# Optimization experiments

Hardware: AMD Instinct MI355X
Metric: run time of the kernel (lower is better)

## Reference

```python
import jax, jax.numpy as jnp
import numpy as np

B, C, D, H, W = 8, 1, 160, 160, 160
SPATIAL_AXES = (2, 3, 4)  # axial, coronal, sagittal map to dims D, H, W


def setup_inputs() -> dict:
    key = jax.random.key(0)
    k1, _ = jax.random.split(key)
    x = jax.random.normal(k1, (B, C, D, H, W), dtype=jnp.float32)
    log_sigma = jnp.zeros((3,), dtype=jnp.float32)  # log(initial_sigma=1.0)
    return {"x": x, "log_sigma": log_sigma}


def reference(x, log_sigma):
    # For each spatial axis: adjacent-slice diff, squared distance summed over
    # channel + remaining spatial dims (per batch, per slice-pair), RBF kernel,
    # then -mean over (batch, slice-pairs). Equivalent to the original
    # sum_i(-mean_b(k_i)) / (n_slices - 1) since mean is linear.
    sigma = jnp.exp(log_sigma)
    total = jnp.float32(0.0)
    for i, ax in enumerate(SPATIAL_AXES):
        d = jnp.diff(x, axis=ax)  # [B, C, ...] with S-1 along ax
        reduce_dims = tuple(a for a in range(5) if a not in (0, ax))
        sq = jnp.sum(d * d, axis=reduce_dims)  # [B, S-1]
        k = jnp.exp(-sq / (2.0 * sigma[i] ** 2))
        total = total + (-jnp.mean(k))
    return total / jnp.float32(len(SPATIAL_AXES))
```

## Files before the change

kernel.cpp:

```cpp
#include <hip/hip_runtime.h>


constexpr int Wd4 = 40;
constexpr int SLICE4 = 6400;
constexpr long BSTR4 = 160L * 6400;
constexpr int NB = 8;
constexpr int ND = 160;
constexpr int NPAIR = 159;
constexpr int NKEY = 3 * NB * NPAIR;
constexpr int BLK_STRIDE = 384;
constexpr int NBLK = NB * ND;
constexpr int PART_OFF = NBLK * BLK_STRIDE;
constexpr int NFIN = 60;

__device__ __forceinline__ float sq4(const float4& a, const float4& c) {
    float e0 = a.x - c.x, e1 = a.y - c.y, e2 = a.z - c.z, e3 = a.w - c.w;
    return e0 * e0 + e1 * e1 + e2 * e2 + e3 * e3;
}

__global__ __launch_bounds__(320) void diff3_kernel(const float* __restrict__ x,
                                                    float* __restrict__ ws) {
    __shared__ float ldsH[20][321];
    __shared__ float accW[160];
    __shared__ float accD;

    const int t = threadIdx.x;
    const int bid = blockIdx.x;
    const int xcd = bid & 7;
    const int idx = bid >> 3;
    const int b = idx / 20;
    const int d = xcd * 20 + idx % 20;
    const bool hasNext = (d < 159);

    const int c4 = t % 40;
    const int r0 = t / 40;
    const bool sOK = (c4 < 39);

    if (t < 160) accW[t] = 0.f;
    if (t == 0)  accD = 0.f;
    __syncthreads();

    const float4* curp = (const float4*)x + (size_t)b * BSTR4 + (size_t)d * SLICE4 + t;
    const float4* nxtp = curp + SLICE4;

    float aW0 = 0.f, aW1 = 0.f, aW2 = 0.f, aW3 = 0.f;
    float aD = 0.f;
    float aH[20];
#pragma unroll
    for (int j = 0; j < 20; ++j) aH[j] = 0.f;

#pragma unroll
    for (int j = 0; j < 20; ++j) {
        const float4 v = curp[320 * j];
        float4 nv;
        if (hasNext) nv = nxtp[320 * j];
        float4 hv;
        const bool hok = (j < 19) || (r0 < 7);
        if (hok) hv = curp[320 * j + Wd4];
        float sb = 0.f;
        if (sOK) sb = ((const float*)(curp + 320 * j))[4];

        float dw;
        dw = v.y - v.x; aW0 += dw * dw;
        dw = v.z - v.y; aW1 += dw * dw;
        dw = v.w - v.z; aW2 += dw * dw;
        if (sOK) { dw = sb - v.w; aW3 += dw * dw; }
        if (hok) aH[j] += sq4(hv, v);
        if (hasNext) aD += sq4(nv, v);
    }

#pragma unroll
    for (int j = 0; j < 20; ++j) ldsH[j][t] = aH[j];
    atomicAdd(&accW[c4 * 4 + 0], aW0);
    atomicAdd(&accW[c4 * 4 + 1], aW1);
    atomicAdd(&accW[c4 * 4 + 2], aW2);
    if (sOK) atomicAdd(&accW[c4 * 4 + 3], aW3);
    if (hasNext) {
        for (int off = 32; off > 0; off >>= 1) aD += __shfl_down(aD, off, 64);
        if ((t & 63) == 0) atomicAdd(&accD, aD);
    }
    __syncthreads();

    float* slot = ws + (size_t)(b * ND + d) * BLK_STRIDE;
    if (t == 0) slot[0] = accD;
    if (t < 160) {
        const int r = t;
        float s = 0.f;
        const float* src = &ldsH[r >> 3][(r & 7) * 40];
        for (int i = 0; i < 40; ++i) s += src[i];
        slot[1 + r] = s;
    }
    if (t >= 160) slot[161 + (t - 160)] = accW[t - 160];
}

__global__ __launch_bounds__(64) void reduce_kernel(const float* __restrict__ ws,
                                                    const float* __restrict__ log_sigma,
                                                    float* __restrict__ part) {
    const int gk = blockIdx.x * 64 + threadIdx.x;
    float kv = 0.f;
    if (gk < NKEY) {
        const int a = gk / (NB * NPAIR);
        const int rem = gk % (NB * NPAIR);
        const int b = rem / NPAIR;
        const int key = rem % NPAIR;
        const float f = -0.5f * expf(-2.f * log_sigma[a]);
        const float* base = ws + (size_t)b * ND * BLK_STRIDE;
        float val;
        if (a == 0) {
            val = base[(size_t)key * BLK_STRIDE];
        } else {
            const int off = (a == 1) ? (1 + key) : (161 + key);
            val = 0.f;
            for (int d2 = 0; d2 < ND; ++d2) val += base[d2 * BLK_STRIDE + off];
        }
        kv = expf(val * f);
    }
    for (int off = 32; off > 0; off >>= 1) kv += __shfl_down(kv, off, 64);
    if (threadIdx.x == 0) part[blockIdx.x] = kv;
}

__global__ __launch_bounds__(64) void final_kernel(const float* __restrict__ part,
                                                   float* __restrict__ out) {
    float v = (threadIdx.x < NFIN) ? part[threadIdx.x] : 0.f;
    for (int off = 32; off > 0; off >>= 1) v += __shfl_down(v, off, 64);
    if (threadIdx.x == 0) out[0] = -v / (float)NKEY;
}

extern "C" void kernel_launch(void* const* d_in, const int* in_sizes, int n_in,
                              void* d_out, int out_size, void* d_ws, size_t ws_size,
                              hipStream_t stream) {
    const float* x = (const float*)d_in[0];
    const float* log_sigma = (const float*)d_in[1];
    float* out = (float*)d_out;
    float* ws = (float*)d_ws;

    diff3_kernel<<<NBLK, 320, 0, stream>>>(x, ws);
    reduce_kernel<<<NFIN, 64, 0, stream>>>(ws, log_sigma, ws + PART_OFF);
    final_kernel<<<1, 64, 0, stream>>>(ws + PART_OFF, out);
}
```

Measured before the change: 236.6 us.

## Tile blocks over 5 depth slices by 32 rows to reuse loads across axes

Each block now covers a 5-slice by 32-row tile instead of one full depth slice. Previous slice and row values are kept in registers, so the depth and height diffs reuse loaded data instead of reloading the next slice and the next row. Width neighbours come through a wave shuffle instead of an unaligned reload. The per-block partial layout shrinks and the reduce kernel is rewritten to sum over the new tiling. The old XCD-aware block remapping is dropped, and tile boundaries still cost one extra slice load and one extra row load.

```diff
diff --git a/kernel.cpp b/kernel.cpp
--- a/kernel.cpp
+++ b/kernel.cpp
@@ -5,12 +5,11 @@
 constexpr int SLICE4 = 6400;
 constexpr long BSTR4 = 160L * 6400;
 constexpr int NB = 8;
-constexpr int ND = 160;
 constexpr int NPAIR = 159;
 constexpr int NKEY = 3 * NB * NPAIR;
-constexpr int BLK_STRIDE = 384;
-constexpr int NBLK = NB * ND;
-constexpr int PART_OFF = NBLK * BLK_STRIDE;
+constexpr int SLOT = 200;
+constexpr int NBLK = NB * 160;
+constexpr int PART_OFF = NBLK * SLOT;
 constexpr int NFIN = 60;
 
 __device__ __forceinline__ float sq4(const float4& a, const float4& c) {
@@ -20,77 +19,116 @@
 
 __global__ __launch_bounds__(320) void diff3_kernel(const float* __restrict__ x,
                                                     float* __restrict__ ws) {
-    __shared__ float ldsH[20][321];
-    __shared__ float accW[160];
-    __shared__ float accD;
+    __shared__ float lds[1504];
 
     const int t = threadIdx.x;
     const int bid = blockIdx.x;
-    const int xcd = bid & 7;
-    const int idx = bid >> 3;
-    const int b = idx / 20;
-    const int d = xcd * 20 + idx % 20;
-    const bool hasNext = (d < 159);
+    const int b = bid / 160;
+    const int r2 = bid % 160;
+    const int ds = r2 / 5;
+    const int hc = r2 % 5;
+    const int d0 = ds * 5, h0 = hc * 32;
+    const bool lastSeg = (ds == 31);
 
     const int c4 = t % 40;
-    const int r0 = t / 40;
+    const int rp = t / 40;
+    const int lane = t & 63;
+    const int wv = t >> 6;
+    const bool hOK = !(hc == 4 && rp == 7);
     const bool sOK = (c4 < 39);
+    const bool fixB = (lane == 63) && sOK;
 
-    if (t < 160) accW[t] = 0.f;
-    if (t == 0)  accD = 0.f;
-    __syncthreads();
+    const float4* base = (const float4*)x + (size_t)b * BSTR4 + (size_t)d0 * SLICE4
+                       + (size_t)(h0 + 4 * rp) * Wd4 + c4;
 
-    const float4* curp = (const float4*)x + (size_t)b * BSTR4 + (size_t)d * SLICE4 + t;
-    const float4* nxtp = curp + SLICE4;
-
-    float aW0 = 0.f, aW1 = 0.f, aW2 = 0.f, aW3 = 0.f;
-    float aD = 0.f;
-    float aH[20];
-#pragma unroll
-    for (int j = 0; j < 20; ++j) aH[j] = 0.f;
+    float aW[4] = {0.f, 0.f, 0.f, 0.f};
+    float aH[4] = {0.f, 0.f, 0.f, 0.f};
+    float aD[5] = {0.f, 0.f, 0.f, 0.f, 0.f};
+    float4 p0, p1, p2, p3;
 
 #pragma unroll
-    for (int j = 0; j < 20; ++j) {
-        const float4 v = curp[320 * j];
-        float4 nv;
-        if (hasNext) nv = nxtp[320 * j];
+    for (int it = 0; it < 5; ++it) {
+        const float4* sp = base + it * SLICE4;
+        const float4 v0 = sp[0];
+        const float4 v1 = sp[Wd4];
+        const float4 v2 = sp[2 * Wd4];
+        const float4 v3 = sp[3 * Wd4];
         float4 hv;
-        const bool hok = (j < 19) || (r0 < 7);
-        if (hok) hv = curp[320 * j + Wd4];
-        float sb = 0.f;
-        if (sOK) sb = ((const float*)(curp + 320 * j))[4];
+        if (hOK) hv = sp[4 * Wd4];
+        float bx0 = 0.f, bx1 = 0.f, bx2 = 0.f, bx3 = 0.f;
+        if (fixB) {
+            bx0 = ((const float*)(sp))[4];
+            bx1 = ((const float*)(sp + Wd4))[4];
+            bx2 = ((const float*)(sp + 2 * Wd4))[4];
+            bx3 = ((const float*)(sp + 3 * Wd4))[4];
+        }
+        float s0 = __shfl_down(v0.x, 1, 64); if (fixB) s0 = bx0;
+        float s1 = __shfl_down(v1.x, 1, 64); if (fixB) s1 = bx1;
+        float s2 = __shfl_down(v2.x, 1, 64); if (fixB) s2 = bx2;
+        float s3 = __shfl_down(v3.x, 1, 64); if (fixB) s3 = bx3;
 
         float dw;
-        dw = v.y - v.x; aW0 += dw * dw;
-        dw = v.z - v.y; aW1 += dw * dw;
-        dw = v.w - v.z; aW2 += dw * dw;
-        if (sOK) { dw = sb - v.w; aW3 += dw * dw; }
-        if (hok) aH[j] += sq4(hv, v);
-        if (hasNext) aD += sq4(nv, v);
+        dw = v0.y - v0.x; aW[0] += dw * dw;
+        dw = v0.z - v0.y; aW[1] += dw * dw;
+        dw = v0.w - v0.z; aW[2] += dw * dw;
+        dw = v1.y - v1.x; aW[0] += dw * dw;
+        dw = v1.z - v1.y; aW[1] += dw * dw;
+        dw = v1.w - v1.z; aW[2] += dw * dw;
+        dw = v2.y - v2.x; aW[0] += dw * dw;
+        dw = v2.z - v2.y; aW[1] += dw * dw;
+        dw = v2.w - v2.z; aW[2] += dw * dw;
+        dw = v3.y - v3.x; aW[0] += dw * dw;
+        dw = v3.z - v3.y; aW[1] += dw * dw;
+        dw = v3.w - v3.z; aW[2] += dw * dw;
+        if (sOK) {
+            dw = s0 - v0.w; aW[3] += dw * dw;
+            dw = s1 - v1.w; aW[3] += dw * dw;
+            dw = s2 - v2.w; aW[3] += dw * dw;
+            dw = s3 - v3.w; aW[3] += dw * dw;
+        }
+        aH[0] += sq4(v1, v0);
+        aH[1] += sq4(v2, v1);
+        aH[2] += sq4(v3, v2);
+        if (hOK) aH[3] += sq4(hv, v3);
+        if (it > 0)
+            aD[it - 1] += sq4(v0, p0) + sq4(v1, p1) + sq4(v2, p2) + sq4(v3, p3);
+        p0 = v0; p1 = v1; p2 = v2; p3 = v3;
+    }
+    if (!lastSeg) {
+        const float4* sp = base + 5 * SLICE4;
+        aD[4] = sq4(sp[0], p0) + sq4(sp[Wd4], p1) + sq4(sp[2 * Wd4], p2) + sq4(sp[3 * Wd4], p3);
     }
 
 #pragma unroll
-    for (int j = 0; j < 20; ++j) ldsH[j][t] = aH[j];
-    atomicAdd(&accW[c4 * 4 + 0], aW0);
-    atomicAdd(&accW[c4 * 4 + 1], aW1);
-    atomicAdd(&accW[c4 * 4 + 2], aW2);
-    if (sOK) atomicAdd(&accW[c4 * 4 + 3], aW3);
-    if (hasNext) {
-        for (int off = 32; off > 0; off >>= 1) aD += __shfl_down(aD, off, 64);
-        if ((t & 63) == 0) atomicAdd(&accD, aD);
+    for (int j = 0; j < 4; ++j) lds[(4 * rp + j) * 41 + c4] = aH[j];
+#pragma unroll
+    for (int j = 0; j < 5; ++j) {
+        float dd = aD[j];
+        for (int off = 32; off > 0; off >>= 1) dd += __shfl_down(dd, off, 64);
+        if (lane == 0) lds[1472 + j * 5 + wv] = dd;
     }
     __syncthreads();
-
-    float* slot = ws + (size_t)(b * ND + d) * BLK_STRIDE;
-    if (t == 0) slot[0] = accD;
+    float hsum = 0.f, dsum = 0.f;
+    if (t < 32) {
+        const float* src = &lds[t * 41];
+        for (int i = 0; i < 40; ++i) hsum += src[i];
+    }
+    if (t < 5) {
+        for (int w2 = 0; w2 < 5; ++w2) dsum += lds[1472 + t * 5 + w2];
+    }
+    __syncthreads();
+#pragma unroll
+    for (int j = 0; j < 4; ++j) lds[(4 * c4 + j) * 9 + rp] = aW[j];
+    __syncthreads();
+    float wsum = 0.f;
     if (t < 160) {
-        const int r = t;
-        float s = 0.f;
-        const float* src = &ldsH[r >> 3][(r & 7) * 40];
-        for (int i = 0; i < 40; ++i) s += src[i];
-        slot[1 + r] = s;
+        const float* src = &lds[t * 9];
+        for (int i = 0; i < 8; ++i) wsum += src[i];
     }
-    if (t >= 160) slot[161 + (t - 160)] = accW[t - 160];
+    float* slot = ws + (size_t)bid * SLOT;
+    if (t < 5)   slot[t] = dsum;
+    if (t < 32)  slot[5 + t] = hsum;
+    if (t < 160) slot[37 + t] = wsum;
 }
 
 __global__ __launch_bounds__(64) void reduce_kernel(const float* __restrict__ ws,
@@ -102,16 +140,21 @@
         const int a = gk / (NB * NPAIR);
         const int rem = gk % (NB * NPAIR);
         const int b = rem / NPAIR;
-        const int key = rem % NPAIR;
+        const int k = rem % NPAIR;
         const float f = -0.5f * expf(-2.f * log_sigma[a]);
-        const float* base = ws + (size_t)b * ND * BLK_STRIDE;
-        float val;
+        const float* bb = ws + (size_t)b * 160 * SLOT;
+        float val = 0.f;
         if (a == 0) {
-            val = base[(size_t)key * BLK_STRIDE];
+            const int ds = k / 5, j = k % 5;
+            const float* p = bb + (size_t)(ds * 5) * SLOT + j;
+            for (int hc = 0; hc < 5; ++hc) val += p[hc * SLOT];
+        } else if (a == 1) {
+            const int hc = k / 32, kk = k % 32;
+            const float* p = bb + (size_t)hc * SLOT + 5 + kk;
+            for (int ds = 0; ds < 32; ++ds) val += p[(size_t)(ds * 5) * SLOT];
         } else {
-            const int off = (a == 1) ? (1 + key) : (161 + key);
-            val = 0.f;
-            for (int d2 = 0; d2 < ND; ++d2) val += base[d2 * BLK_STRIDE + off];
+            const float* p = bb + 37 + k;
+            for (int i = 0; i < 160; ++i) val += p[(size_t)i * SLOT];
         }
         kv = expf(val * f);
     }
```

New measurement: 197.1 us (median of 2 runs). 16.7% less time.
